# Optimization experiments

Hardware: AMD Instinct MI355X
Metric: run time of the kernel (lower is better)

## Reference

```python
import jax
import jax.numpy as jnp
from jax import lax
import numpy as np

B, C, H, W = 16, 96, 112, 112
HIDDEN = 4 * C
LN_EPS = 1e-6  # ConvNeXt LayerNorm eps


def setup_inputs() -> dict:
    key = jax.random.key(0)
    ks = jax.random.split(key, 8)
    x = jax.random.normal(ks[0], (B, C, H, W), dtype=jnp.float32)
    # depthwise 7x7 kernel, HWIO with feature_group_count=C -> (7,7,1,C)
    dw_w = jax.random.normal(ks[1], (7, 7, 1, C), dtype=jnp.float32) * 0.02
    dw_b = jnp.zeros((C,), dtype=jnp.float32)
    gamma = jnp.ones((C,), dtype=jnp.float32)
    beta = jnp.zeros((C,), dtype=jnp.float32)
    w1 = jax.random.normal(ks[2], (C, HIDDEN), dtype=jnp.float32) * 0.02
    b1 = jnp.zeros((HIDDEN,), dtype=jnp.float32)
    w2 = jax.random.normal(ks[3], (HIDDEN, C), dtype=jnp.float32) * 0.02
    b2 = jnp.zeros((C,), dtype=jnp.float32)
    scale = jnp.full((C,), 1e-6, dtype=jnp.float32)  # block_scale init 1e-6
    return {"x": x, "dw_w": dw_w, "dw_b": dw_b, "gamma": gamma, "beta": beta,
            "w1": w1, "b1": b1, "w2": w2, "b2": b2, "scale": scale}


def reference(x, dw_w, dw_b, gamma, beta, w1, b1, w2, b2, scale):
    # depthwise 7x7, stride 1, padding 3 (SAME), groups = C
    y = lax.conv_general_dilated(
        x, dw_w, window_strides=(1, 1), padding="SAME",
        dimension_numbers=("NCHW", "HWIO", "NCHW"),
        feature_group_count=C,
    ) + dw_b[None, :, None, None]
    # BCHW -> BHWC
    y = jnp.transpose(y, (0, 2, 3, 1))
    # LayerNorm over channel dim
    mu = jnp.mean(y, axis=-1, keepdims=True)
    var = jnp.var(y, axis=-1, keepdims=True)
    y = (y - mu) * lax.rsqrt(var + LN_EPS) * gamma + beta
    # pointwise MLP with exact GELU (torch nn.GELU default)
    h = jax.nn.gelu(jnp.einsum("bhwc,cd->bhwd", y, w1) + b1, approximate=False)
    y = jnp.einsum("bhwd,dc->bhwc", h, w2) + b2
    # BHWC -> BCHW, scale, residual (eval mode: stochastic depth = identity)
    y = jnp.transpose(y, (0, 3, 1, 2))
    return scale[None, :, None, None] * y + x
```

## Files before the change

### kernel.cpp

```cpp
#include <hip/hip_runtime.h>
#include <hip/hip_bf16.h>

#define BATCH 16
#define CCH 96
#define HH 112
#define WW 112
#define HID 384
#define NPIX (BATCH * HH * WW)
#define HW (HH * WW)

#define PXB 64
#define ZROWD 50
#define SLICE_B 12288
#define RING_B (2 * SLICE_B)
#define B1_OFF RING_B
#define SMEM_TOTAL (RING_B + 1536)

#define XSTR 132

typedef __attribute__((ext_vector_type(8))) short bf16x8;
typedef __attribute__((ext_vector_type(4))) float f32x4;
typedef __attribute__((ext_vector_type(4))) unsigned int uint4v;

typedef const __attribute__((address_space(1))) void gvoid_t;
typedef __attribute__((address_space(3))) void svoid_t;

__device__ __forceinline__ short f2bf(float v) {
    __hip_bfloat16 h = __float2bfloat16(v);
    return __builtin_bit_cast(short, h);
}
__device__ __forceinline__ float bf2f(short s) {
    unsigned int u = ((unsigned int)(unsigned short)s) << 16;
    return __builtin_bit_cast(float, u);
}
__device__ __forceinline__ float gelu_fast(float v) {
    float e = __expf(-1.702f * v);
    return v * __builtin_amdgcn_rcpf(1.0f + e);
}

__global__ __launch_bounds__(256) void pack_w(const float* __restrict__ w1,
                                              const float* __restrict__ w2,
                                              const float* __restrict__ gamma,
                                              const float* __restrict__ scale,
                                              short* __restrict__ wp) {
    int o = blockIdx.x * 256 + threadIdx.x;
    if (o >= 12 * 12 * 64 * 8) return;
    const int j   = o & 7;
    const int l   = (o >> 3) & 63;
    const int g   = o >> 9;
    const int f   = g % 12;
    const int kk2 = g / 12;
    float v;
    if (f < 6) {
        const int kk = f >> 1, mh = f & 1;
        const int c  = kk * 32 + (l >> 4) * 8 + j;
        const int d  = (2 * kk2 + mh) * 16 + (l & 15);
        v = gamma[c] * w1[c * HID + d];
    } else {
        const int nt2 = f - 6;
        const int dd  = kk2 * 32 + ((j >> 2) << 4) + ((l >> 4) << 2) + (j & 3);
        const int n   = nt2 * 16 + (l & 15);
        v = w2[dd * CCH + n] * scale[n];
    }
    wp[o] = f2bf(v);
}

__global__ __launch_bounds__(256) void pack_bias(const float* __restrict__ w1,
                                                 const float* __restrict__ b1,
                                                 const float* __restrict__ beta,
                                                 const float* __restrict__ b2,
                                                 const float* __restrict__ scale,
                                                 float* __restrict__ b1p,
                                                 float* __restrict__ b2p) {
    int t = blockIdx.x * 256 + threadIdx.x;
    if (t < HID) {
        float s = b1[t];
        for (int c = 0; c < CCH; ++c) s += beta[c] * w1[c * HID + t];
        b1p[t] = s;
    } else if (t < HID + CCH) {
        int c = t - HID;
        b2p[c] = scale[c] * b2[c];
    }
}

__global__ __launch_bounds__(256) void conv_kernel(
    const float* __restrict__ x, const float* __restrict__ dww,
    const float* __restrict__ dwb, short* __restrict__ y)
{
    __shared__ float xs[34 * XSTR];

    const int t = threadIdx.x;
    const int p = blockIdx.x;
    int o = (p & 7) * 768 + (p >> 3);
    const int ht = o & 3;  o >>= 2;
    const int c  = o % CCH;
    const int b  = o / CCH;
    const int h0 = ht * 28;
    const float* xc = x + (size_t)(b * CCH + c) * HW;

    float4 vbuf[5];
    #pragma unroll
    for (int k = 0; k < 5; ++k) {
        const int idx = t + 256 * k;
        const int r  = idx >> 5;
        const int j  = idx & 31;
        const int gh = h0 - 3 + r;
        float4 v = make_float4(0.f, 0.f, 0.f, 0.f);
        if (idx < 1088 && (unsigned)gh < HH && j >= 1 && j <= 28)
            v = *reinterpret_cast<const float4*>(xc + gh * WW + 4 * j - 4);
        vbuf[k] = v;
    }
    #pragma unroll
    for (int k = 0; k < 5; ++k) {
        const int idx = t + 256 * k;
        if (idx < 1088)
            *reinterpret_cast<float4*>(&xs[(idx >> 5) * XSTR + (idx & 31) * 4]) = vbuf[k];
    }
    __syncthreads();

    const int wg = t >> 5;
    const int r  = t & 31;
    if (wg < 7 && r < 28) {
        const int j0 = wg * 16;
        const float bias = dwb[c];
        float acc[16];
        #pragma unroll
        for (int i = 0; i < 16; ++i) acc[i] = bias;
        #pragma unroll
        for (int kh = 0; kh < 7; ++kh) {
            f32x4 qd[6];
            #pragma unroll
            for (int u = 0; u < 6; ++u)
                qd[u] = *reinterpret_cast<const f32x4*>(&xs[(r + kh) * XSTR + j0 + 4 * u]);
            #pragma unroll
            for (int kw = 0; kw < 7; ++kw) {
                const float wt = dww[(kh * 7 + kw) * CCH + c];
                #pragma unroll
                for (int i = 0; i < 16; ++i) {
                    const int jj = i + kw + 1;
                    acc[i] += qd[jj >> 2][jj & 3] * wt;
                }
            }
        }
        uint4v w0, w1v;
        #pragma unroll
        for (int u = 0; u < 4; ++u) {
            w0[u]  = (unsigned int)(unsigned short)f2bf(acc[2 * u]) |
                     ((unsigned int)(unsigned short)f2bf(acc[2 * u + 1]) << 16);
            w1v[u] = (unsigned int)(unsigned short)f2bf(acc[8 + 2 * u]) |
                     ((unsigned int)(unsigned short)f2bf(acc[9 + 2 * u]) << 16);
        }
        short* yc = y + (size_t)(b * CCH + c) * HW + (h0 + r) * WW + j0;
        *reinterpret_cast<uint4v*>(yc)     = w0;
        *reinterpret_cast<uint4v*>(yc + 8) = w1v;
    }
}

__global__ __launch_bounds__(128) void mlp_kernel(
    const short* __restrict__ ybuf, const char* __restrict__ wp,
    const float* __restrict__ b1p, const float* __restrict__ b2p,
    const float* __restrict__ x, float* __restrict__ out)
{
    __shared__ __align__(16) char smem[SMEM_TOTAL];
    unsigned int* zr = (unsigned int*)smem;
    float* b1l = (float*)(smem + B1_OFF);

    const int t    = threadIdx.x;
    const int lane = t & 63;
    const int wv   = t >> 6;
    const int l15  = lane & 15;
    const int q    = lane >> 4;
    const int px0  = blockIdx.x * PXB;
    const int b    = px0 / HW;
    const int hw0  = px0 - b * HW;

    if (t < 96) {
        const int pxq = t / 48;
        const int cp  = t - pxq * 48;
        const unsigned int* Ap = (const unsigned int*)(ybuf +
            (size_t)(b * CCH + 2 * cp) * HW + hw0 + pxq * 32);
        const unsigned int* Bp = (const unsigned int*)(ybuf +
            (size_t)(b * CCH + 2 * cp + 1) * HW + hw0 + pxq * 32);
        #pragma unroll
        for (int e = 0; e < 4; ++e) {
            const uint4v A  = *reinterpret_cast<const uint4v*>(Ap + e * 4);
            const uint4v Bv = *reinterpret_cast<const uint4v*>(Bp + e * 4);
            #pragma unroll
            for (int k = 0; k < 4; ++k) {
                const int px = pxq * 32 + e * 8 + 2 * k;
                zr[px * ZROWD + cp]       = (A[k] & 0xffffu) | (Bv[k] << 16);
                zr[(px + 1) * ZROWD + cp] = (A[k] >> 16) | (Bv[k] & 0xffff0000u);
            }
        }
    } else {
        const int i0 = (t - 96) * 12;
        #pragma unroll
        for (int i2 = 0; i2 < 12; ++i2) b1l[i0 + i2] = b1p[i0 + i2];
    }

    f32x4 acc2[2][6];
    #pragma unroll
    for (int nt2 = 0; nt2 < 6; ++nt2) {
        const int c = nt2 * 16 + l15;
        const float bv = b2p[c];
        #pragma unroll
        for (int m2 = 0; m2 < 2; ++m2) {
            const size_t g = (size_t)(b * CCH + c) * HW + hw0 + wv * 32 + m2 * 16 + q * 4;
            const f32x4 xv = *reinterpret_cast<const f32x4*>(x + g);
            acc2[m2][nt2].x = bv + xv.x;  acc2[m2][nt2].y = bv + xv.y;
            acc2[m2][nt2].z = bv + xv.z;  acc2[m2][nt2].w = bv + xv.w;
        }
    }
    __syncthreads();

    bf16x8 za[2][3];
    #pragma unroll
    for (int nt = 0; nt < 2; ++nt) {
        const int row = wv * 32 + nt * 16 + l15;
        const char* base = smem + row * (ZROWD * 4) + q * 16;
        float s1 = 0.f, s2 = 0.f;
        #pragma unroll
        for (int kk = 0; kk < 3; ++kk) {
            za[nt][kk] = *reinterpret_cast<const bf16x8*>(base + kk * 64);
            #pragma unroll
            for (int j = 0; j < 8; ++j) {
                const float v = bf2f(za[nt][kk][j]);
                s1 += v; s2 += v * v;
            }
        }
        s1 += __shfl_xor(s1, 16, 64);  s2 += __shfl_xor(s2, 16, 64);
        s1 += __shfl_xor(s1, 32, 64);  s2 += __shfl_xor(s2, 32, 64);
        const float mu   = s1 * (1.0f / CCH);
        const float rstd = rsqrtf(s2 * (1.0f / CCH) - mu * mu + 1e-6f);
        #pragma unroll
        for (int kk = 0; kk < 3; ++kk)
            #pragma unroll
            for (int j = 0; j < 8; ++j)
                za[nt][kk][j] = f2bf((bf2f(za[nt][kk][j]) - mu) * rstd);
    }
    __syncthreads();

    asm volatile("s_waitcnt vmcnt(0)" ::: "memory");

    #define STAGE_F(SL, SLOT)                                                       \
        {                                                                           \
            const char* _s = wp + (size_t)(SL) * SLICE_B + (wv * 6) * 1024 +        \
                             lane * 16;                                             \
            char* _d = smem + (SLOT) * SLICE_B + (wv * 6) * 1024;                   \
            __builtin_amdgcn_global_load_lds((gvoid_t*)(_s),        (svoid_t*)(_d),        16, 0, 0); \
            __builtin_amdgcn_global_load_lds((gvoid_t*)(_s + 1024), (svoid_t*)(_d + 1024), 16, 0, 0); \
            __builtin_amdgcn_global_load_lds((gvoid_t*)(_s + 2048), (svoid_t*)(_d + 2048), 16, 0, 0); \
            __builtin_amdgcn_global_load_lds((gvoid_t*)(_s + 3072), (svoid_t*)(_d + 3072), 16, 0, 0); \
            __builtin_amdgcn_global_load_lds((gvoid_t*)(_s + 4096), (svoid_t*)(_d + 4096), 16, 0, 0); \
            __builtin_amdgcn_global_load_lds((gvoid_t*)(_s + 5120), (svoid_t*)(_d + 5120), 16, 0, 0); \
        }

    STAGE_F(0, 0);

    #pragma unroll
    for (int kk2 = 0; kk2 < 12; ++kk2) {
        asm volatile("s_waitcnt vmcnt(0)" ::: "memory");
        __builtin_amdgcn_s_barrier();
        __builtin_amdgcn_sched_barrier(0);
        if (kk2 < 11) STAGE_F(kk2 + 1, (kk2 + 1) & 1);

        const char* wb = smem + (kk2 & 1) * SLICE_B + lane * 16;

        f32x4 p0[2], p1[2];
        const f32x4 bva = *reinterpret_cast<const f32x4*>(b1l + 32 * kk2 + q * 4);
        const f32x4 bvb = *reinterpret_cast<const f32x4*>(b1l + 32 * kk2 + 16 + q * 4);
        p0[0] = bva;  p0[1] = bva;
        p1[0] = bvb;  p1[1] = bvb;
        #pragma unroll
        for (int kk = 0; kk < 3; ++kk) {
            const bf16x8 wfa = *reinterpret_cast<const bf16x8*>(wb + (kk * 2) * 1024);
            const bf16x8 wfb = *reinterpret_cast<const bf16x8*>(wb + (kk * 2 + 1) * 1024);
            p0[0] = __builtin_amdgcn_mfma_f32_16x16x32_bf16(wfa, za[0][kk], p0[0], 0, 0, 0);
            p0[1] = __builtin_amdgcn_mfma_f32_16x16x32_bf16(wfa, za[1][kk], p0[1], 0, 0, 0);
            p1[0] = __builtin_amdgcn_mfma_f32_16x16x32_bf16(wfb, za[0][kk], p1[0], 0, 0, 0);
            p1[1] = __builtin_amdgcn_mfma_f32_16x16x32_bf16(wfb, za[1][kk], p1[1], 0, 0, 0);
        }
        bf16x8 hv[2];
        #pragma unroll
        for (int nt = 0; nt < 2; ++nt)
            #pragma unroll
            for (int i = 0; i < 4; ++i) {
                hv[nt][i]     = f2bf(gelu_fast(p0[nt][i]));
                hv[nt][4 + i] = f2bf(gelu_fast(p1[nt][i]));
            }
        #pragma unroll
        for (int nt2 = 0; nt2 < 6; ++nt2) {
            const bf16x8 bfr = *reinterpret_cast<const bf16x8*>(wb + (6 + nt2) * 1024);
            acc2[0][nt2] = __builtin_amdgcn_mfma_f32_16x16x32_bf16(hv[0], bfr, acc2[0][nt2], 0, 0, 0);
            acc2[1][nt2] = __builtin_amdgcn_mfma_f32_16x16x32_bf16(hv[1], bfr, acc2[1][nt2], 0, 0, 0);
        }
    }
    #undef STAGE_F

    #pragma unroll
    for (int m2 = 0; m2 < 2; ++m2) {
        const int pxl = hw0 + wv * 32 + m2 * 16 + q * 4;
        #pragma unroll
        for (int nt2 = 0; nt2 < 6; ++nt2) {
            const int c = nt2 * 16 + l15;
            const size_t g = (size_t)(b * CCH + c) * HW + pxl;
            *reinterpret_cast<f32x4*>(out + g) = acc2[m2][nt2];
        }
    }
}

extern "C" void kernel_launch(void* const* d_in, const int* in_sizes, int n_in,
                              void* d_out, int out_size, void* d_ws, size_t ws_size,
                              hipStream_t stream) {
    const float* x     = (const float*)d_in[0];
    const float* dww   = (const float*)d_in[1];
    const float* dwb   = (const float*)d_in[2];
    const float* gamma = (const float*)d_in[3];
    const float* beta  = (const float*)d_in[4];
    const float* w1    = (const float*)d_in[5];
    const float* b1    = (const float*)d_in[6];
    const float* w2    = (const float*)d_in[7];
    const float* b2    = (const float*)d_in[8];
    const float* scale = (const float*)d_in[9];
    float* out = (float*)d_out;

    char* ws = (char*)d_ws;
    short* ybuf = (short*)ws;
    const size_t Y_BYTES = (size_t)NPIX * CCH * 2;
    short* wp  = (short*)(ws + Y_BYTES);
    float* b1p = (float*)(ws + Y_BYTES + 12 * SLICE_B);
    float* b2p = b1p + HID;

    pack_w<<<(12 * 12 * 64 * 8 + 255) / 256, 256, 0, stream>>>(w1, w2, gamma, scale, wp);
    pack_bias<<<2, 256, 0, stream>>>(w1, b1, beta, b2, scale, b1p, b2p);
    conv_kernel<<<BATCH * CCH * 4, 256, 0, stream>>>(x, dww, dwb, ybuf);
    mlp_kernel<<<NPIX / PXB, 128, 0, stream>>>(ybuf, (const char*)wp, b1p, b2p, x, out);
}
```

Measured before the change: 124.2 us.

## Enlarge MLP blocks to 256 pixels and use three-slot weight ring

Each MLP block now handles 256 pixels with 512 threads instead of 64 pixels with 128 threads, so each staged weight slice is shared by four times as many pixels. This cuts global/L2 weight traffic per pixel. The weight ring becomes three slots, and the next slice is issued before a partial vmcnt wait and barrier, so weight loads overlap compute. The ring reuses the LDS area of the transposed activations. The tighter launch bound (512, 2) may force register spills, and fewer, larger blocks reduce scheduling flexibility.

```diff
diff --git a/kernel.cpp b/kernel.cpp
--- a/kernel.cpp
+++ b/kernel.cpp
@@ -9,12 +9,13 @@
 #define NPIX (BATCH * HH * WW)
 #define HW (HH * WW)
 
-#define PXB 64
+#define PXB 256
 #define ZROWD 50
 #define SLICE_B 12288
-#define RING_B (2 * SLICE_B)
-#define B1_OFF RING_B
-#define SMEM_TOTAL (RING_B + 1536)
+#define RING_SLOTS 3
+#define ZR_BYTES (PXB * ZROWD * 4)
+#define B1_OFF ZR_BYTES
+#define SMEM_TOTAL (ZR_BYTES + 1536)
 
 #define XSTR 132
 
@@ -156,7 +157,7 @@
     }
 }
 
-__global__ __launch_bounds__(128) void mlp_kernel(
+__global__ __launch_bounds__(512, 2) void mlp_kernel(
     const short* __restrict__ ybuf, const char* __restrict__ wp,
     const float* __restrict__ b1p, const float* __restrict__ b2p,
     const float* __restrict__ x, float* __restrict__ out)
@@ -174,7 +175,7 @@
     const int b    = px0 / HW;
     const int hw0  = px0 - b * HW;
 
-    if (t < 96) {
+    if (t < 384) {
         const int pxq = t / 48;
         const int cp  = t - pxq * 48;
         const unsigned int* Ap = (const unsigned int*)(ybuf +
@@ -193,9 +194,9 @@
             }
         }
     } else {
-        const int i0 = (t - 96) * 12;
-        #pragma unroll
-        for (int i2 = 0; i2 < 12; ++i2) b1l[i0 + i2] = b1p[i0 + i2];
+        const int i0 = (t - 384) * 3;
+        #pragma unroll
+        for (int i2 = 0; i2 < 3; ++i2) b1l[i0 + i2] = b1p[i0 + i2];
     }
 
     f32x4 acc2[2][6];
@@ -243,28 +244,30 @@
     asm volatile("s_waitcnt vmcnt(0)" ::: "memory");
 
     #define STAGE_F(SL, SLOT)                                                       \
-        {                                                                           \
-            const char* _s = wp + (size_t)(SL) * SLICE_B + (wv * 6) * 1024 +        \
+        if (wv < 6) {                                                               \
+            const char* _s = wp + (size_t)(SL) * SLICE_B + (wv * 2) * 1024 +        \
                              lane * 16;                                             \
-            char* _d = smem + (SLOT) * SLICE_B + (wv * 6) * 1024;                   \
+            char* _d = smem + (SLOT) * SLICE_B + (wv * 2) * 1024;                   \
             __builtin_amdgcn_global_load_lds((gvoid_t*)(_s),        (svoid_t*)(_d),        16, 0, 0); \
             __builtin_amdgcn_global_load_lds((gvoid_t*)(_s + 1024), (svoid_t*)(_d + 1024), 16, 0, 0); \
-            __builtin_amdgcn_global_load_lds((gvoid_t*)(_s + 2048), (svoid_t*)(_d + 2048), 16, 0, 0); \
-            __builtin_amdgcn_global_load_lds((gvoid_t*)(_s + 3072), (svoid_t*)(_d + 3072), 16, 0, 0); \
-            __builtin_amdgcn_global_load_lds((gvoid_t*)(_s + 4096), (svoid_t*)(_d + 4096), 16, 0, 0); \
-            __builtin_amdgcn_global_load_lds((gvoid_t*)(_s + 5120), (svoid_t*)(_d + 5120), 16, 0, 0); \
+        }
+    #define WAITBAR()                                                               \
+        {                                                                           \
+            asm volatile("s_waitcnt vmcnt(2)" ::: "memory");                        \
+            __builtin_amdgcn_s_barrier();                                           \
+            __builtin_amdgcn_sched_barrier(0);                                      \
         }
 
     STAGE_F(0, 0);
 
     #pragma unroll
     for (int kk2 = 0; kk2 < 12; ++kk2) {
-        asm volatile("s_waitcnt vmcnt(0)" ::: "memory");
-        __builtin_amdgcn_s_barrier();
-        __builtin_amdgcn_sched_barrier(0);
-        if (kk2 < 11) STAGE_F(kk2 + 1, (kk2 + 1) & 1);
-
-        const char* wb = smem + (kk2 & 1) * SLICE_B + lane * 16;
+        {
+            const int sl = (kk2 + 1 > 11) ? 11 : kk2 + 1;
+            STAGE_F(sl, sl % RING_SLOTS);
+        }
+        WAITBAR();
+        const char* wb = smem + (kk2 % RING_SLOTS) * SLICE_B + lane * 16;
 
         f32x4 p0[2], p1[2];
         const f32x4 bva = *reinterpret_cast<const f32x4*>(b1l + 32 * kk2 + q * 4);
@@ -296,6 +299,7 @@
         }
     }
     #undef STAGE_F
+    #undef WAITBAR
 
     #pragma unroll
     for (int m2 = 0; m2 < 2; ++m2) {
@@ -334,5 +338,5 @@
     pack_w<<<(12 * 12 * 64 * 8 + 255) / 256, 256, 0, stream>>>(w1, w2, gamma, scale, wp);
     pack_bias<<<2, 256, 0, stream>>>(w1, b1, beta, b2, scale, b1p, b2p);
     conv_kernel<<<BATCH * CCH * 4, 256, 0, stream>>>(x, dww, dwb, ybuf);
-    mlp_kernel<<<NPIX / PXB, 128, 0, stream>>>(ybuf, (const char*)wp, b1p, b2p, x, out);
-}
+    mlp_kernel<<<NPIX / PXB, 512, 0, stream>>>(ybuf, (const char*)wp, b1p, b2p, x, out);
+}
```

Measured after the change: 143.9 us. 1.16x slower.
